# Kernel optimization log

Measured on AMD Instinct MI355X. Metric: run time of the kernel, lower is better.

## Reference

```python
import jax, jax.numpy as jnp
import numpy as np

B, N, FIN, FOUT = 8, 2048, 128, 128


def setup_inputs() -> dict:
    key = jax.random.key(0)
    k1, k2, k3, k4, k5 = jax.random.split(key, 5)
    x = jax.random.normal(k1, (B, N, FIN), dtype=jnp.float32)
    adj = jax.random.randint(k2, (N, N), 0, 2, dtype=jnp.int32)
    # W stored [in, out] (transpose of torch Linear weight; same math via x @ W)
    W = jax.random.normal(k3, (FIN, FOUT), dtype=jnp.float32) * (1.0 / np.sqrt(FIN))
    # a: Linear(2*out, 1) split into src/dst halves: a([h_i,h_j]) = h_i@a_src + h_j@a_dst
    a_src = jax.random.normal(k4, (FOUT,), dtype=jnp.float32) * 0.1
    a_dst = jax.random.normal(k5, (FOUT,), dtype=jnp.float32) * 0.1
    return {"x": x, "adj": adj, "W": W, "a_src": a_src, "a_dst": a_dst}


def reference(x, adj, W, a_src, a_dst):
    # h: [B, N, FOUT]
    h = jnp.einsum('bnf,fo->bno', x, W)
    # attention logits e_ij = LeakyReLU(a_src.h_i + a_dst.h_j), built by broadcast
    s_i = jnp.einsum('bno,o->bn', h, a_src)  # [B, N]
    s_j = jnp.einsum('bno,o->bn', h, a_dst)  # [B, N]
    e = jax.nn.leaky_relu(s_i[:, :, None] + s_j[:, None, :], negative_slope=0.2)  # [B,N,N]
    scores = jnp.where(adj[None, :, :] == 0, -jnp.inf, e)
    attn = jax.nn.softmax(scores, axis=-1)
    attn = jnp.nan_to_num(attn, nan=0.0)  # rows with no neighbors -> all zeros
    # dropout is identity in eval mode
    out = jnp.einsum('bij,bjo->bio', attn, h)  # [B, N, FOUT]
    return out
```

## Files before the change

kernel.cpp:

```cpp
#include <hip/hip_runtime.h>
#include <math.h>

#define BATCH 8
#define NN 2048
#define FF 128

typedef __attribute__((ext_vector_type(4))) float f32x4;
typedef _Float16 half8 __attribute__((ext_vector_type(8)));

__device__ __forceinline__ unsigned short h2u(_Float16 h) {
    return __builtin_bit_cast(unsigned short, h);
}

__device__ __forceinline__ void h_split(float f, unsigned short& hi, unsigned short& lo) {
    const _Float16 hh = (_Float16)f;
    hi = h2u(hh);
    lo = h2u((_Float16)(f - (float)hh));
}

__global__ __launch_bounds__(512) void k_prep(const int* __restrict__ adj,
                                              const float* __restrict__ W,
                                              unsigned short* __restrict__ Wf_hi,
                                              unsigned short* __restrict__ Wf_lo,
                                              unsigned* __restrict__ amT) {
    const int t = threadIdx.x;
    if (blockIdx.x == 128) {
        #pragma unroll 4
        for (int e = 0; e < 32; ++e) {
            const int fi = e * 512 + t;
            const int j = fi & 7, lane = (fi >> 3) & 63, nt = (fi >> 9) & 7, ks = fi >> 12;
            const int k = ks * 32 + (lane >> 4) * 8 + j;
            const int col = nt * 16 + (lane & 15);
            unsigned short hh, hl;
            h_split(W[k * FF + col], hh, hl);
            Wf_hi[fi] = hh;
            Wf_lo[fi] = hl;
        }
    } else {
        const int w = t >> 6, lane = t & 63;
        const int row = blockIdx.x * 16 + w * 2;
        #pragma unroll
        for (int rr = 0; rr < 2; ++rr) {
            const int* __restrict__ ar = adj + (size_t)(row + rr) * NN;
            for (int seg = 0; seg < 32; ++seg) {
                const unsigned long long m = __ballot(ar[seg * 64 + lane] != 0);
                if (lane == 0)  amT[(size_t)(seg * 2) * NN + row + rr] = (unsigned)m;
                if (lane == 32) amT[(size_t)(seg * 2 + 1) * NN + row + rr] = (unsigned)(m >> 32);
            }
        }
    }
}

__global__ __launch_bounds__(512) void k_h(const float* __restrict__ x,
                                           const unsigned short* __restrict__ Wf_hi,
                                           const unsigned short* __restrict__ Wf_lo,
                                           const float* __restrict__ a_src,
                                           const float* __restrict__ a_dst,
                                           unsigned short* __restrict__ hF,
                                           float* __restrict__ Eg,  float* __restrict__ E2g,
                                           float* __restrict__ Sg,  float* __restrict__ S2g) {
    __shared__ float sred[2][64];
    __shared__ float dred[2][64];

    const int t = threadIdx.x;
    const int w = t >> 6, lane = t & 63;
    const int mt = w >> 1, ch = w & 1;
    const int nl = lane & 15, quad = lane >> 4;
    const int row0 = blockIdx.x * 64;
    const int b = row0 >> 11, jloc0 = row0 & 2047;
    const int gr = row0 + mt * 16 + nl;

    f32x4 acc[4] = {{0.f,0.f,0.f,0.f},{0.f,0.f,0.f,0.f},{0.f,0.f,0.f,0.f},{0.f,0.f,0.f,0.f}};

    #pragma unroll
    for (int ks = 0; ks < 4; ++ks) {
        const float4 xa = *reinterpret_cast<const float4*>(&x[(size_t)gr * FF + ks * 32 + quad * 8]);
        const float4 xb = *reinterpret_cast<const float4*>(&x[(size_t)gr * FF + ks * 32 + quad * 8 + 4]);
        const float xv[8] = {xa.x, xa.y, xa.z, xa.w, xb.x, xb.y, xb.z, xb.w};
        half8 ah, al;
        #pragma unroll
        for (int i = 0; i < 8; ++i) {
            const _Float16 hh = (_Float16)xv[i];
            ah[i] = hh;
            al[i] = (_Float16)(xv[i] - (float)hh);
        }
        #pragma unroll
        for (int nt = 0; nt < 4; ++nt) {
            const int gnt = ch * 4 + nt;
            const int bo = ((ks * 8 + gnt) * 64 + lane) * 8;
            const half8 bh = *reinterpret_cast<const half8*>(&Wf_hi[bo]);
            const half8 bl = *reinterpret_cast<const half8*>(&Wf_lo[bo]);
            acc[nt] = __builtin_amdgcn_mfma_f32_16x16x32_f16(ah, bh, acc[nt], 0, 0, 0);
            acc[nt] = __builtin_amdgcn_mfma_f32_16x16x32_f16(al, bh, acc[nt], 0, 0, 0);
            acc[nt] = __builtin_amdgcn_mfma_f32_16x16x32_f16(ah, bl, acc[nt], 0, 0, 0);
        }
    }

    const int jloc = jloc0 + mt * 16 + quad * 4;
    const int jg = jloc >> 3, u0 = jloc & 7;
    #pragma unroll
    for (int nt = 0; nt < 4; ++nt) {
        const int gnt = ch * 4 + nt;
        ushort4 hv;
        hv.x = h2u((_Float16)acc[nt][0]);
        hv.y = h2u((_Float16)acc[nt][1]);
        hv.z = h2u((_Float16)acc[nt][2]);
        hv.w = h2u((_Float16)acc[nt][3]);
        *reinterpret_cast<ushort4*>(&hF[(size_t)b * 262144 + gnt * 32768 + jg * 128 + nl * 8 + u0]) = hv;
    }

    float as[4], ad[4];
    #pragma unroll
    for (int nt = 0; nt < 4; ++nt) {
        const int col = ch * 64 + nt * 16 + nl;
        as[nt] = a_src[col];
        ad[nt] = a_dst[col];
    }
    #pragma unroll
    for (int r = 0; r < 4; ++r) {
        float sp = acc[0][r] * as[0] + acc[1][r] * as[1] + acc[2][r] * as[2] + acc[3][r] * as[3];
        float dp = acc[0][r] * ad[0] + acc[1][r] * ad[1] + acc[2][r] * ad[2] + acc[3][r] * ad[3];
        #pragma unroll
        for (int off = 8; off >= 1; off >>= 1) {
            sp += __shfl_xor(sp, off, 16);
            dp += __shfl_xor(dp, off, 16);
        }
        if (nl == 0) {
            sred[ch][mt * 16 + quad * 4 + r] = sp;
            dred[ch][mt * 16 + quad * 4 + r] = dp;
        }
    }
    __syncthreads();
    if (t < 64) {
        const float sp = sred[0][t] + sred[1][t];
        const float dp = dred[0][t] + dred[1][t];
        const int row = row0 + t;
        Sg[row]  = __expf(sp - 2.f);
        S2g[row] = __expf(0.2f * sp - 2.f);
        Eg[row]  = __expf(dp - 2.f);
        E2g[row] = __expf(0.2f * dp - 2.f);
    }
}

__global__ __launch_bounds__(512) void k_attn(const unsigned short* __restrict__ hF,
                                              const unsigned* __restrict__ amT,
                                              const float* __restrict__ Eg,
                                              const float* __restrict__ E2g,
                                              const float* __restrict__ Sg,
                                              const float* __restrict__ S2g,
                                              float* __restrict__ out) {
    __shared__ float E_l[NN];
    __shared__ float E2_l[NN];
    __shared__ unsigned am_l[64 * 64];
    __shared__ unsigned short pA_hi[2][64 * 72];
    __shared__ unsigned short pA_lo[2][64 * 72];
    __shared__ float l_s[64];

    const int t = threadIdx.x;
    const int b = blockIdx.y;
    const int i0 = blockIdx.x * 64;

    *reinterpret_cast<float4*>(&E_l[t * 4])  = *reinterpret_cast<const float4*>(&Eg[(size_t)b * NN + t * 4]);
    *reinterpret_cast<float4*>(&E2_l[t * 4]) = *reinterpret_cast<const float4*>(&E2g[(size_t)b * NN + t * 4]);
    #pragma unroll
    for (int k = 0; k < 8; ++k) {
        const int idx = k * 512 + t;
        am_l[idx] = amT[(size_t)(idx >> 6) * NN + i0 + (idx & 63)];
    }
    __syncthreads();

    const int rp = t >> 4, jw4 = t & 15;
    const int ra = rp * 2, rb = ra + 1;
    const float2 eia = make_float2(Sg[(size_t)b * NN + i0 + ra], S2g[(size_t)b * NN + i0 + ra]);
    const float2 eib = make_float2(Sg[(size_t)b * NN + i0 + rb], S2g[(size_t)b * NN + i0 + rb]);
    const int bitb = (jw4 & 7) * 4;
    const int pwo = ra * 72 + jw4 * 4;

    const int w = t >> 6, lane = t & 63;
    const int mt = w >> 1, ch = w & 1;
    const int nl = lane & 15, quad = lane >> 4;
    const unsigned short* __restrict__ hFb = hF + (size_t)b * 262144;
    int bofs[4];
    #pragma unroll
    for (int nt = 0; nt < 4; ++nt)
        bofs[nt] = (ch * 4 + nt) * 32768 + quad * 128 + nl * 8;
    const int aofs = (mt * 16 + nl) * 72 + quad * 8;

    f32x4 acc[4] = {{0.f,0.f,0.f,0.f},{0.f,0.f,0.f,0.f},{0.f,0.f,0.f,0.f},{0.f,0.f,0.f,0.f}};
    float la = 0.f, lb = 0.f;

    for (int tt = 0; tt < 32; ++tt) {
        const int jt = tt * 64;
        const int buf = tt & 1;
        const int jofs = jt * 16;

        half8 bfr[4][2];
        #pragma unroll
        for (int nt = 0; nt < 4; ++nt) {
            bfr[nt][0] = *reinterpret_cast<const half8*>(hFb + bofs[nt] + jofs);
            bfr[nt][1] = *reinterpret_cast<const half8*>(hFb + bofs[nt] + jofs + 512);
        }

        {
            const int jb = jt + jw4 * 4;
            const float4 ej4  = *reinterpret_cast<const float4*>(&E_l[jb]);
            const float4 e2j4 = *reinterpret_cast<const float4*>(&E2_l[jb]);
            const uint2 mw = *reinterpret_cast<const uint2*>(&am_l[(tt * 2 + (jw4 >> 3)) * 64 + ra]);
            const float ejA[4]  = {ej4.x, ej4.y, ej4.z, ej4.w};
            const float e2jA[4] = {e2j4.x, e2j4.y, e2j4.z, e2j4.w};
            float pa[4], pb[4];
            #pragma unroll
            for (int jj = 0; jj < 4; ++jj) {
                const float ua = fmaxf(eia.x * ejA[jj], eia.y * e2jA[jj]);
                const float ub = fmaxf(eib.x * ejA[jj], eib.y * e2jA[jj]);
                pa[jj] = ((mw.x >> (bitb + jj)) & 1u) ? ua : 0.f;
                pb[jj] = ((mw.y >> (bitb + jj)) & 1u) ? ub : 0.f;
                la += pa[jj];
                lb += pb[jj];
            }
            ushort4 hv, lv;
            h_split(pa[0], hv.x, lv.x);
            h_split(pa[1], hv.y, lv.y);
            h_split(pa[2], hv.z, lv.z);
            h_split(pa[3], hv.w, lv.w);
            *reinterpret_cast<ushort4*>(&pA_hi[buf][pwo]) = hv;
            *reinterpret_cast<ushort4*>(&pA_lo[buf][pwo]) = lv;
            h_split(pb[0], hv.x, lv.x);
            h_split(pb[1], hv.y, lv.y);
            h_split(pb[2], hv.z, lv.z);
            h_split(pb[3], hv.w, lv.w);
            *reinterpret_cast<ushort4*>(&pA_hi[buf][pwo + 72]) = hv;
            *reinterpret_cast<ushort4*>(&pA_lo[buf][pwo + 72]) = lv;
        }

        __syncthreads();

        const half8 ah0 = *reinterpret_cast<const half8*>(&pA_hi[buf][aofs]);
        const half8 ah1 = *reinterpret_cast<const half8*>(&pA_hi[buf][aofs + 32]);
        const half8 al0 = *reinterpret_cast<const half8*>(&pA_lo[buf][aofs]);
        const half8 al1 = *reinterpret_cast<const half8*>(&pA_lo[buf][aofs + 32]);
        #pragma unroll
        for (int nt = 0; nt < 4; ++nt) {
            acc[nt] = __builtin_amdgcn_mfma_f32_16x16x32_f16(ah0, bfr[nt][0], acc[nt], 0, 0, 0);
            acc[nt] = __builtin_amdgcn_mfma_f32_16x16x32_f16(al0, bfr[nt][0], acc[nt], 0, 0, 0);
            acc[nt] = __builtin_amdgcn_mfma_f32_16x16x32_f16(ah1, bfr[nt][1], acc[nt], 0, 0, 0);
            acc[nt] = __builtin_amdgcn_mfma_f32_16x16x32_f16(al1, bfr[nt][1], acc[nt], 0, 0, 0);
        }
    }

    #pragma unroll
    for (int off = 8; off >= 1; off >>= 1) {
        la += __shfl_xor(la, off, 16);
        lb += __shfl_xor(lb, off, 16);
    }
    if (jw4 == 0) {
        l_s[ra] = la;
        l_s[rb] = lb;
    }
    __syncthreads();
    if (t < 64) {
        const float l = l_s[t];
        l_s[t] = (l > 0.f) ? 1.f / l : 0.f;
    }
    __syncthreads();

    const int col0 = ch * 64 + nl;
    #pragma unroll
    for (int nt = 0; nt < 4; ++nt) {
        #pragma unroll
        for (int r = 0; r < 4; ++r) {
            const int lrow = mt * 16 + quad * 4 + r;
            out[((size_t)b * NN + i0 + lrow) * FF + col0 + nt * 16] = acc[nt][r] * l_s[lrow];
        }
    }
}

extern "C" void kernel_launch(void* const* d_in, const int* in_sizes, int n_in,
                              void* d_out, int out_size, void* d_ws, size_t ws_size,
                              hipStream_t stream) {
    const float* x     = (const float*)d_in[0];
    const int*   adj   = (const int*)d_in[1];
    const float* W     = (const float*)d_in[2];
    const float* a_src = (const float*)d_in[3];
    const float* a_dst = (const float*)d_in[4];
    float* out = (float*)d_out;

    unsigned short* hF    = (unsigned short*)d_ws;
    unsigned short* Wf_hi = hF + 2097152;
    unsigned short* Wf_lo = Wf_hi + 16384;
    float* Eg  = (float*)(Wf_lo + 16384);
    float* E2g = Eg + 16384;
    float* Sg  = E2g + 16384;
    float* S2g = Sg + 16384;
    unsigned* amT = (unsigned*)(S2g + 16384);

    k_prep<<<129, 512, 0, stream>>>(adj, W, Wf_hi, Wf_lo, amT);
    k_h<<<256, 512, 0, stream>>>(x, Wf_hi, Wf_lo, a_src, a_dst, hF, Eg, E2g, Sg, S2g);
    k_attn<<<dim3(NN / 64, BATCH), 512, 0, stream>>>(hF, amT, Eg, E2g, Sg, S2g, out);
}
```

Measured before the change: 131.5 us.

## Drop fp16 hi/lo split of attention probabilities and sum rows via MFMA

The attention kernel no longer splits each probability into fp16 hi and lo parts. A single fp16 P tile now feeds the MFMAs, which halves both the MFMA count for the P·h product and the LDS traffic for the P tiles. The row-sum normalizer is computed by an extra MFMA against a ones vector instead of scalar accumulation plus a shuffle reduction and LDS pass. The warp tiling is re-arranged to a 2x2 M/N split, launch bounds request 2 blocks per CU, and the adjacency-packing loop is unrolled. The risk is lower accuracy, since probabilities are rounded to fp16 without a residual term.

```diff
diff --git a/kernel.cpp b/kernel.cpp
--- a/kernel.cpp
+++ b/kernel.cpp
@@ -42,6 +42,7 @@
         #pragma unroll
         for (int rr = 0; rr < 2; ++rr) {
             const int* __restrict__ ar = adj + (size_t)(row + rr) * NN;
+            #pragma unroll 16
             for (int seg = 0; seg < 32; ++seg) {
                 const unsigned long long m = __ballot(ar[seg * 64 + lane] != 0);
                 if (lane == 0)  amT[(size_t)(seg * 2) * NN + row + rr] = (unsigned)m;
@@ -142,19 +143,17 @@
     }
 }
 
-__global__ __launch_bounds__(512) void k_attn(const unsigned short* __restrict__ hF,
-                                              const unsigned* __restrict__ amT,
-                                              const float* __restrict__ Eg,
-                                              const float* __restrict__ E2g,
-                                              const float* __restrict__ Sg,
-                                              const float* __restrict__ S2g,
-                                              float* __restrict__ out) {
+__global__ __launch_bounds__(512, 2) void k_attn(const unsigned short* __restrict__ hF,
+                                                 const unsigned* __restrict__ amT,
+                                                 const float* __restrict__ Eg,
+                                                 const float* __restrict__ E2g,
+                                                 const float* __restrict__ Sg,
+                                                 const float* __restrict__ S2g,
+                                                 float* __restrict__ out) {
     __shared__ float E_l[NN];
     __shared__ float E2_l[NN];
     __shared__ unsigned am_l[64 * 64];
-    __shared__ unsigned short pA_hi[2][64 * 72];
-    __shared__ unsigned short pA_lo[2][64 * 72];
-    __shared__ float l_s[64];
+    __shared__ unsigned short pA[2][64 * 72];
 
     const int t = threadIdx.x;
     const int b = blockIdx.y;
@@ -171,34 +170,39 @@
 
     const int rp = t >> 4, jw4 = t & 15;
     const int ra = rp * 2, rb = ra + 1;
-    const float2 eia = make_float2(Sg[(size_t)b * NN + i0 + ra], S2g[(size_t)b * NN + i0 + ra]);
-    const float2 eib = make_float2(Sg[(size_t)b * NN + i0 + rb], S2g[(size_t)b * NN + i0 + rb]);
+    const float Sa  = Sg[(size_t)b * NN + i0 + ra];
+    const float S2a = S2g[(size_t)b * NN + i0 + ra];
+    const float Sb  = Sg[(size_t)b * NN + i0 + rb];
+    const float S2b = S2g[(size_t)b * NN + i0 + rb];
     const int bitb = (jw4 & 7) * 4;
     const int pwo = ra * 72 + jw4 * 4;
 
     const int w = t >> 6, lane = t & 63;
-    const int mt = w >> 1, ch = w & 1;
     const int nl = lane & 15, quad = lane >> 4;
+    const int mtp = w & 1, ntp = w >> 1;
     const unsigned short* __restrict__ hFb = hF + (size_t)b * 262144;
-    int bofs[4];
-    #pragma unroll
-    for (int nt = 0; nt < 4; ++nt)
-        bofs[nt] = (ch * 4 + nt) * 32768 + quad * 128 + nl * 8;
-    const int aofs = (mt * 16 + nl) * 72 + quad * 8;
-
-    f32x4 acc[4] = {{0.f,0.f,0.f,0.f},{0.f,0.f,0.f,0.f},{0.f,0.f,0.f,0.f},{0.f,0.f,0.f,0.f}};
-    float la = 0.f, lb = 0.f;
+    int bofs[2], aofs[2];
+    #pragma unroll
+    for (int nn = 0; nn < 2; ++nn) bofs[nn] = (ntp + nn * 4) * 32768 + quad * 128 + nl * 8;
+    #pragma unroll
+    for (int mm = 0; mm < 2; ++mm) aofs[mm] = ((mtp + mm * 2) * 16 + nl) * 72 + quad * 8;
+
+    f32x4 acc[2][2] = {{{0.f,0.f,0.f,0.f},{0.f,0.f,0.f,0.f}},{{0.f,0.f,0.f,0.f},{0.f,0.f,0.f,0.f}}};
+    f32x4 lac[2] = {{0.f,0.f,0.f,0.f},{0.f,0.f,0.f,0.f}};
+    half8 ones;
+    #pragma unroll
+    for (int i = 0; i < 8; ++i) ones[i] = (_Float16)1.f;
 
     for (int tt = 0; tt < 32; ++tt) {
         const int jt = tt * 64;
         const int buf = tt & 1;
         const int jofs = jt * 16;
 
-        half8 bfr[4][2];
-        #pragma unroll
-        for (int nt = 0; nt < 4; ++nt) {
-            bfr[nt][0] = *reinterpret_cast<const half8*>(hFb + bofs[nt] + jofs);
-            bfr[nt][1] = *reinterpret_cast<const half8*>(hFb + bofs[nt] + jofs + 512);
+        half8 bfr[2][2];
+        #pragma unroll
+        for (int nn = 0; nn < 2; ++nn) {
+            bfr[nn][0] = *reinterpret_cast<const half8*>(hFb + bofs[nn] + jofs);
+            bfr[nn][1] = *reinterpret_cast<const half8*>(hFb + bofs[nn] + jofs + 512);
         }
 
         {
@@ -208,69 +212,51 @@
             const uint2 mw = *reinterpret_cast<const uint2*>(&am_l[(tt * 2 + (jw4 >> 3)) * 64 + ra]);
             const float ejA[4]  = {ej4.x, ej4.y, ej4.z, ej4.w};
             const float e2jA[4] = {e2j4.x, e2j4.y, e2j4.z, e2j4.w};
-            float pa[4], pb[4];
+            ushort4 ha, hb;
             #pragma unroll
             for (int jj = 0; jj < 4; ++jj) {
-                const float ua = fmaxf(eia.x * ejA[jj], eia.y * e2jA[jj]);
-                const float ub = fmaxf(eib.x * ejA[jj], eib.y * e2jA[jj]);
-                pa[jj] = ((mw.x >> (bitb + jj)) & 1u) ? ua : 0.f;
-                pb[jj] = ((mw.y >> (bitb + jj)) & 1u) ? ub : 0.f;
-                la += pa[jj];
-                lb += pb[jj];
-            }
-            ushort4 hv, lv;
-            h_split(pa[0], hv.x, lv.x);
-            h_split(pa[1], hv.y, lv.y);
-            h_split(pa[2], hv.z, lv.z);
-            h_split(pa[3], hv.w, lv.w);
-            *reinterpret_cast<ushort4*>(&pA_hi[buf][pwo]) = hv;
-            *reinterpret_cast<ushort4*>(&pA_lo[buf][pwo]) = lv;
-            h_split(pb[0], hv.x, lv.x);
-            h_split(pb[1], hv.y, lv.y);
-            h_split(pb[2], hv.z, lv.z);
-            h_split(pb[3], hv.w, lv.w);
-            *reinterpret_cast<ushort4*>(&pA_hi[buf][pwo + 72]) = hv;
-            *reinterpret_cast<ushort4*>(&pA_lo[buf][pwo + 72]) = lv;
+                const float ua = fmaxf(Sa * ejA[jj], S2a * e2jA[jj]);
+                const float ub = fmaxf(Sb * ejA[jj], S2b * e2jA[jj]);
+                const float pa = ((mw.x >> (bitb + jj)) & 1u) ? ua : 0.f;
+                const float pb = ((mw.y >> (bitb + jj)) & 1u) ? ub : 0.f;
+                ((unsigned short*)&ha)[jj] = h2u((_Float16)pa);
+                ((unsigned short*)&hb)[jj] = h2u((_Float16)pb);
+            }
+            *reinterpret_cast<ushort4*>(&pA[buf][pwo]) = ha;
+            *reinterpret_cast<ushort4*>(&pA[buf][pwo + 72]) = hb;
         }
 
         __syncthreads();
 
-        const half8 ah0 = *reinterpret_cast<const half8*>(&pA_hi[buf][aofs]);
-        const half8 ah1 = *reinterpret_cast<const half8*>(&pA_hi[buf][aofs + 32]);
-        const half8 al0 = *reinterpret_cast<const half8*>(&pA_lo[buf][aofs]);
-        const half8 al1 = *reinterpret_cast<const half8*>(&pA_lo[buf][aofs + 32]);
-        #pragma unroll
-        for (int nt = 0; nt < 4; ++nt) {
-            acc[nt] = __builtin_amdgcn_mfma_f32_16x16x32_f16(ah0, bfr[nt][0], acc[nt], 0, 0, 0);
-            acc[nt] = __builtin_amdgcn_mfma_f32_16x16x32_f16(al0, bfr[nt][0], acc[nt], 0, 0, 0);
-            acc[nt] = __builtin_amdgcn_mfma_f32_16x16x32_f16(ah1, bfr[nt][1], acc[nt], 0, 0, 0);
-            acc[nt] = __builtin_amdgcn_mfma_f32_16x16x32_f16(al1, bfr[nt][1], acc[nt], 0, 0, 0);
-        }
-    }
-
-    #pragma unroll
-    for (int off = 8; off >= 1; off >>= 1) {
-        la += __shfl_xor(la, off, 16);
-        lb += __shfl_xor(lb, off, 16);
-    }
-    if (jw4 == 0) {
-        l_s[ra] = la;
-        l_s[rb] = lb;
-    }
-    __syncthreads();
-    if (t < 64) {
-        const float l = l_s[t];
-        l_s[t] = (l > 0.f) ? 1.f / l : 0.f;
-    }
-    __syncthreads();
-
-    const int col0 = ch * 64 + nl;
-    #pragma unroll
-    for (int nt = 0; nt < 4; ++nt) {
+        half8 afr[2][2];
+        #pragma unroll
+        for (int mm = 0; mm < 2; ++mm) {
+            afr[mm][0] = *reinterpret_cast<const half8*>(&pA[buf][aofs[mm]]);
+            afr[mm][1] = *reinterpret_cast<const half8*>(&pA[buf][aofs[mm] + 32]);
+        }
+        #pragma unroll
+        for (int mm = 0; mm < 2; ++mm) {
+            #pragma unroll
+            for (int kh = 0; kh < 2; ++kh) {
+                lac[mm] = __builtin_amdgcn_mfma_f32_16x16x32_f16(afr[mm][kh], ones, lac[mm], 0, 0, 0);
+                acc[mm][0] = __builtin_amdgcn_mfma_f32_16x16x32_f16(afr[mm][kh], bfr[0][kh], acc[mm][0], 0, 0, 0);
+                acc[mm][1] = __builtin_amdgcn_mfma_f32_16x16x32_f16(afr[mm][kh], bfr[1][kh], acc[mm][1], 0, 0, 0);
+            }
+        }
+    }
+
+    #pragma unroll
+    for (int mm = 0; mm < 2; ++mm) {
+        const int row = i0 + (mtp + mm * 2) * 16 + quad * 4;
         #pragma unroll
         for (int r = 0; r < 4; ++r) {
-            const int lrow = mt * 16 + quad * 4 + r;
-            out[((size_t)b * NN + i0 + lrow) * FF + col0 + nt * 16] = acc[nt][r] * l_s[lrow];
+            const float l = lac[mm][r];
+            const float inv = (l > 0.f) ? 1.f / l : 0.f;
+            #pragma unroll
+            for (int nn = 0; nn < 2; ++nn) {
+                const int col = (ntp + nn * 4) * 16 + nl;
+                out[((size_t)b * NN + row + r) * FF + col] = acc[mm][nn][r] * inv;
+            }
         }
     }
 }
```

Result: faster. 124.2 us (-5.5%).
